# Performance work log

Hardware: AMD Instinct MI355X
Metric: run time of the kernel (lower is better)

Reference implementation:

```python
import jax, jax.numpy as jnp
import numpy as np

N, E = 50000, 800000
IN_DIM, HID, OUT = 64, 128, 64
EPS = 1e-5  # BatchNorm eps


def setup_inputs() -> dict:
    key = jax.random.key(0)
    ks = jax.random.split(key, 16)
    def w(k, i, o):
        return jax.random.normal(k, (i, o), jnp.float32) / np.float32(np.sqrt(i))
    def bn(k):
        km, kv = jax.random.split(k)
        return (jnp.ones((HID,), jnp.float32),                       # gamma
                jnp.zeros((HID,), jnp.float32),                      # beta
                0.1 * jax.random.normal(km, (HID,), jnp.float32),    # running mean
                0.5 + jax.random.uniform(kv, (HID,), jnp.float32))   # running var
    g0, be0, m0, v0 = bn(ks[6])
    g1, be1, m1, v1 = bn(ks[7])
    g2, be2, m2, v2 = bn(ks[8])
    return {
        "x":   jax.random.normal(ks[0], (N, IN_DIM), jnp.float32),
        "src": jax.random.randint(ks[1], (E,), 0, N, jnp.int32),
        "dst": jax.random.randint(ks[2], (E,), 0, N, jnp.int32),
        "W0": w(ks[3], IN_DIM, HID), "b0": jnp.zeros((HID,), jnp.float32),
        "g0": g0, "be0": be0, "m0": m0, "v0": v0,
        "W1": w(ks[4], HID, HID), "b1": jnp.zeros((HID,), jnp.float32),
        "g1": g1, "be1": be1, "m1": m1, "v1": v1,
        "W2": w(ks[5], HID, HID), "b2": jnp.zeros((HID,), jnp.float32),
        "g2": g2, "be2": be2, "m2": m2, "v2": v2,
        "Wm1": w(ks[9], HID, HID), "bm1": jnp.zeros((HID,), jnp.float32),
        "Wm2": w(ks[10], HID, OUT), "bm2": jnp.zeros((OUT,), jnp.float32),
    }


def gcn_conv(x, src, dst, W, b):
    # PyG GCNConv: h = x @ W; add self loops; symmetric normalization; scatter-add; + bias
    h = x @ W                                                     # [N, F]
    ones = jnp.ones((src.shape[0],), h.dtype)
    deg = 1.0 + jax.ops.segment_sum(ones, dst, num_segments=N)   # self loop adds 1
    dinv = jax.lax.rsqrt(deg)                                     # deg^-1/2 (deg >= 1)
    coef = (dinv[src] * dinv[dst])[:, None]                       # per-edge norm
    agg = jax.ops.segment_sum(h[src] * coef, dst, num_segments=N)
    return agg + h * (dinv * dinv)[:, None] + b                   # self-loop term + bias


def bn_relu(x, g, be, m, v):
    # eval-mode BatchNorm1d followed by ReLU (dropout is identity in eval)
    return jax.nn.relu((x - m) * jax.lax.rsqrt(v + EPS) * g + be)


def reference(x, src, dst,
              W0, b0, g0, be0, m0, v0,
              W1, b1, g1, be1, m1, v1,
              W2, b2, g2, be2, m2, v2,
              Wm1, bm1, Wm2, bm2):
    h = bn_relu(gcn_conv(x, src, dst, W0, b0), g0, be0, m0, v0)
    h = bn_relu(gcn_conv(h, src, dst, W1, b1), g1, be1, m1, v1)
    h = bn_relu(gcn_conv(h, src, dst, W2, b2), g2, be2, m2, v2)
    h = jax.nn.relu(h @ Wm1 + bm1)
    return h @ Wm2 + bm2
```

## Files before the change

### kernel.cpp

```cpp
#include <hip/hip_runtime.h>
#include <hip/hip_fp16.h>

#define BN_EPS 1e-5f
#define BK 512
#define NBMAX 128
#define ECH 8192
#define BCAP 9216
#define ECAP 64

typedef _Float16 half_t;
typedef _Float16 half8 __attribute__((ext_vector_type(8)));
typedef float floatx4 __attribute__((ext_vector_type(4)));


__global__ __launch_bounds__(256) void scatter_cvt_kernel(
    const int* __restrict__ src, const int* __restrict__ dst,
    int* __restrict__ bcursor, int2* __restrict__ tmp,
    const float* __restrict__ x, __half* __restrict__ x16,
    int E, int nb, int sb, int n4) {
  const int t = threadIdx.x;
  if (blockIdx.x >= sb) {
    int i = (blockIdx.x - sb) * 256 + t;
    if (i < n4) {
      float4 v = *(const float4*)(x + (size_t)i * 4);
      union { __half h[4]; float2 f; } u;
      u.h[0] = __float2half_rn(v.x);
      u.h[1] = __float2half_rn(v.y);
      u.h[2] = __float2half_rn(v.z);
      u.h[3] = __float2half_rn(v.w);
      *(float2*)(x16 + (size_t)i * 4) = u.f;
    }
    return;
  }
  __shared__ int h[NBMAX];
  for (int i = t; i < nb; i += 256) h[i] = 0;
  __syncthreads();
  const int base = blockIdx.x * ECH;
#pragma unroll 8
  for (int p = 0; p < ECH / 256; ++p) {
    int e = base + p * 256 + t;
    if (e < E) atomicAdd(&h[dst[e] >> 9], 1);
  }
  __syncthreads();
  for (int i = t; i < nb; i += 256) {
    int c = h[i];
    h[i] = c ? (i * BCAP + atomicAdd(&bcursor[i], c)) : 0;
  }
  __syncthreads();
#pragma unroll 8
  for (int p = 0; p < ECH / 256; ++p) {
    int e = base + p * 256 + t;
    if (e < E) {
      int s = src[e], d = dst[e];
      int pos = atomicAdd(&h[d >> 9], 1);
      tmp[pos] = make_int2(s, d);
    }
  }
}

__global__ __launch_bounds__(256) void bucket_finalize_kernel(
    const int2* __restrict__ tmp, const int* __restrict__ bcursor,
    int* __restrict__ offs, int* __restrict__ offe, float* __restrict__ dinv,
    int* __restrict__ esrc, __half* __restrict__ x16, int n) {
  __shared__ int deg[BK];
  __shared__ int cur[BK];
  __shared__ float fdi[BK];
  __shared__ int ts[256];
  const int t = threadIdx.x;
  const int b = blockIdx.x;
  const int nbase = b * BK;
  const int nn = min(BK, n - nbase);
  const int cnt = bcursor[b];
  const int2* tp = tmp + (size_t)b * BCAP;
  for (int i = t; i < nn; i += 256) deg[i] = 0;
  __syncthreads();
  for (int e = t; e < cnt; e += 256)
    atomicAdd(&deg[tp[e].y - nbase], 1);
  __syncthreads();
  int d0 = (2 * t < nn) ? deg[2 * t] : 0;
  int d1 = (2 * t + 1 < nn) ? deg[2 * t + 1] : 0;
  ts[t] = d0 + d1;
  __syncthreads();
  for (int o = 1; o < 256; o <<= 1) {
    int v = (t >= o) ? ts[t - o] : 0;
    __syncthreads();
    ts[t] += v;
    __syncthreads();
  }
  int base = b * BCAP + ((t == 0) ? 0 : ts[t - 1]);
  if (2 * t < nn) {
    float di = rsqrtf(1.0f + (float)d0);
    offs[nbase + 2 * t] = base;
    offe[nbase + 2 * t] = base + d0;
    cur[2 * t] = base;
    fdi[2 * t] = di;
    dinv[nbase + 2 * t] = di;
  }
  if (2 * t + 1 < nn) {
    float di = rsqrtf(1.0f + (float)d1);
    offs[nbase + 2 * t + 1] = base + d0;
    offe[nbase + 2 * t + 1] = base + d0 + d1;
    cur[2 * t + 1] = base + d0;
    fdi[2 * t + 1] = di;
    dinv[nbase + 2 * t + 1] = di;
  }
  __syncthreads();
  for (int e = t; e < cnt; e += 256) {
    int2 r = tp[e];
    int pos = atomicAdd(&cur[r.y - nbase], 1);
    esrc[pos] = r.x;
  }
  __half2* xp = (__half2*)x16;
  for (int i = t; i < nn * 32; i += 256) {
    int nl = i >> 5;
    size_t idx = (((size_t)(nbase + nl)) << 5) + (i & 31);
    float2 v = __half22float2(xp[idx]);
    float s = fdi[nl];
    xp[idx] = __floats2half2_rn(v.x * s, v.y * s);
  }
}


template <int FIN, int FOUT, int EPI, bool HALFOUT>
__global__ __launch_bounds__(256) void mgemm_kernel(
    const __half* __restrict__ X, const float* __restrict__ W,
    const float* __restrict__ bias, const float* __restrict__ gam,
    const float* __restrict__ bet, const float* __restrict__ mean,
    const float* __restrict__ var, void* __restrict__ Yv, int n) {
  constexpr int LDK = 72;
  constexpr int NCI = FOUT / 16;
  __shared__ half_t Asm[128 * LDK];
  __shared__ half_t Bsm[FOUT * LDK];

  const int t = threadIdx.x;
  const int wave = t >> 6, lane = t & 63;
  const int quad = lane >> 4, l16 = lane & 15;
  const int rowBase = blockIdx.x * 128;

  floatx4 acc[2][NCI];
#pragma unroll
  for (int i = 0; i < 2; ++i)
#pragma unroll
    for (int ci = 0; ci < NCI; ++ci) acc[i][ci] = (floatx4){0.f, 0.f, 0.f, 0.f};

  for (int kc = 0; kc < FIN; kc += 64) {
    __syncthreads();
    {
      const int kq = t & 15, m0 = t >> 4;
#pragma unroll
      for (int p = 0; p < 8; ++p) {
        int m = p * 16 + m0;
        int row = rowBase + m;
        uint2 v = make_uint2(0u, 0u);
        if (row < n) v = *(const uint2*)(X + (size_t)row * FIN + kc + kq * 4);
        *(uint2*)&Asm[m * LDK + kq * 4] = v;
      }
    }
    {
#pragma unroll
      for (int c0 = 0; c0 < FOUT * 16; c0 += 256) {
        int c = c0 + t;
        int nn = c % FOUT;
        int kg = (c / FOUT) * 4;
        const float* wp = W + (size_t)(kc + kg) * FOUT + nn;
        half_t* d = &Bsm[nn * LDK + kg];
        d[0] = (half_t)wp[0];
        d[1] = (half_t)wp[FOUT];
        d[2] = (half_t)wp[2 * FOUT];
        d[3] = (half_t)wp[3 * FOUT];
      }
    }
    __syncthreads();
#pragma unroll
    for (int kk = 0; kk < 2; ++kk) {
      half8 a0 = *(const half8*)&Asm[(wave * 32 + l16) * LDK + kk * 32 + quad * 8];
      half8 a1 = *(const half8*)&Asm[(wave * 32 + 16 + l16) * LDK + kk * 32 + quad * 8];
#pragma unroll
      for (int ci = 0; ci < NCI; ++ci) {
        half8 b = *(const half8*)&Bsm[(ci * 16 + l16) * LDK + kk * 32 + quad * 8];
        acc[0][ci] = __builtin_amdgcn_mfma_f32_16x16x32_f16(a0, b, acc[0][ci], 0, 0, 0);
        acc[1][ci] = __builtin_amdgcn_mfma_f32_16x16x32_f16(a1, b, acc[1][ci], 0, 0, 0);
      }
    }
  }

  float sc[NCI], sh[NCI];
#pragma unroll
  for (int ci = 0; ci < NCI; ++ci) {
    int col = ci * 16 + l16;
    if constexpr (EPI == 3) {
      float s = gam[col] * rsqrtf(var[col] + BN_EPS);
      sc[ci] = s;
      sh[ci] = (bias[col] - mean[col]) * s + bet[col];
    } else if constexpr (EPI == 1 || EPI == 2) {
      sc[ci] = 1.f;
      sh[ci] = bias[col];
    } else {
      sc[ci] = 1.f;
      sh[ci] = 0.f;
    }
  }
  float rs[2][4];
  if constexpr (EPI == 4) {
#pragma unroll
    for (int ri = 0; ri < 2; ++ri)
#pragma unroll
      for (int r = 0; r < 4; ++r) {
        int row = rowBase + wave * 32 + ri * 16 + quad * 4 + r;
        rs[ri][r] = (row < n) ? bias[row] : 0.f;
      }
  }
#pragma unroll
  for (int ri = 0; ri < 2; ++ri)
#pragma unroll
    for (int ci = 0; ci < NCI; ++ci) {
      int col = ci * 16 + l16;
#pragma unroll
      for (int r = 0; r < 4; ++r) {
        int row = rowBase + wave * 32 + ri * 16 + quad * 4 + r;
        if (row < n) {
          float v = acc[ri][ci][r];
          if constexpr (EPI == 4) v *= rs[ri][r];
          if constexpr (EPI == 1 || EPI == 2 || EPI == 3) v = fmaf(v, sc[ci], sh[ci]);
          if constexpr (EPI == 1 || EPI == 3) v = fmaxf(v, 0.f);
          if constexpr (HALFOUT)
            ((half_t*)Yv)[(size_t)row * FOUT + col] = (half_t)v;
          else
            ((float*)Yv)[(size_t)row * FOUT + col] = v;
        }
      }
    }
}


__global__ __launch_bounds__(256) void mlp_kernel(
    const __half* __restrict__ X, const float* __restrict__ W1,
    const float* __restrict__ b1f, const float* __restrict__ W2,
    const float* __restrict__ b2f, float* __restrict__ Y, int n) {
  constexpr int LDK = 72;
  constexpr int LDK2 = 136;
  __shared__ half_t smem[(128 + 64) * LDK2];
  half_t* As1 = smem;
  half_t* Bs1 = smem + 128 * LDK;
  half_t* As2 = smem;
  half_t* Bs2 = smem + 128 * LDK2;

  const int t = threadIdx.x;
  const int wave = t >> 6, lane = t & 63;
  const int quad = lane >> 4, l16 = lane & 15;
  const int rowBase = blockIdx.x * 128;

  floatx4 acc[2][8];
#pragma unroll
  for (int i = 0; i < 2; ++i)
#pragma unroll
    for (int ci = 0; ci < 8; ++ci) acc[i][ci] = (floatx4){0.f, 0.f, 0.f, 0.f};

  for (int kc = 0; kc < 128; kc += 64) {
    __syncthreads();
    {
      const int kq = t & 15, m0 = t >> 4;
#pragma unroll
      for (int p = 0; p < 8; ++p) {
        int m = p * 16 + m0;
        int row = rowBase + m;
        uint2 v = make_uint2(0u, 0u);
        if (row < n) v = *(const uint2*)(X + (size_t)row * 128 + kc + kq * 4);
        *(uint2*)&As1[m * LDK + kq * 4] = v;
      }
    }
    {
#pragma unroll
      for (int c0 = 0; c0 < 128 * 16; c0 += 256) {
        int c = c0 + t;
        int nn = c & 127;
        int kg = (c >> 7) << 2;
        const float* wp = W1 + (size_t)(kc + kg) * 128 + nn;
        half_t* d = &Bs1[nn * LDK + kg];
        d[0] = (half_t)wp[0];
        d[1] = (half_t)wp[128];
        d[2] = (half_t)wp[256];
        d[3] = (half_t)wp[384];
      }
    }
    __syncthreads();
#pragma unroll
    for (int kk = 0; kk < 2; ++kk) {
      half8 a0 = *(const half8*)&As1[(wave * 32 + l16) * LDK + kk * 32 + quad * 8];
      half8 a1 = *(const half8*)&As1[(wave * 32 + 16 + l16) * LDK + kk * 32 + quad * 8];
#pragma unroll
      for (int ci = 0; ci < 8; ++ci) {
        half8 b = *(const half8*)&Bs1[(ci * 16 + l16) * LDK + kk * 32 + quad * 8];
        acc[0][ci] = __builtin_amdgcn_mfma_f32_16x16x32_f16(a0, b, acc[0][ci], 0, 0, 0);
        acc[1][ci] = __builtin_amdgcn_mfma_f32_16x16x32_f16(a1, b, acc[1][ci], 0, 0, 0);
      }
    }
  }
  __syncthreads();

#pragma unroll
  for (int ri = 0; ri < 2; ++ri)
#pragma unroll
    for (int ci = 0; ci < 8; ++ci) {
      int col = ci * 16 + l16;
      float bz = b1f[col];
#pragma unroll
      for (int r = 0; r < 4; ++r) {
        int m = wave * 32 + ri * 16 + quad * 4 + r;
        As2[m * LDK2 + col] = (half_t)fmaxf(acc[ri][ci][r] + bz, 0.f);
      }
    }
  {
#pragma unroll
    for (int c0 = 0; c0 < 64 * 32; c0 += 256) {
      int c = c0 + t;
      int nn = c & 63;
      int kg = (c >> 6) << 2;
      const float* wp = W2 + (size_t)kg * 64 + nn;
      half_t* d = &Bs2[nn * LDK2 + kg];
      d[0] = (half_t)wp[0];
      d[1] = (half_t)wp[64];
      d[2] = (half_t)wp[128];
      d[3] = (half_t)wp[192];
    }
  }
  __syncthreads();

  floatx4 acc2[2][4];
#pragma unroll
  for (int i = 0; i < 2; ++i)
#pragma unroll
    for (int ci = 0; ci < 4; ++ci) acc2[i][ci] = (floatx4){0.f, 0.f, 0.f, 0.f};
#pragma unroll
  for (int kk = 0; kk < 4; ++kk) {
    half8 a0 = *(const half8*)&As2[(wave * 32 + l16) * LDK2 + kk * 32 + quad * 8];
    half8 a1 = *(const half8*)&As2[(wave * 32 + 16 + l16) * LDK2 + kk * 32 + quad * 8];
#pragma unroll
    for (int ci = 0; ci < 4; ++ci) {
      half8 b = *(const half8*)&Bs2[(ci * 16 + l16) * LDK2 + kk * 32 + quad * 8];
      acc2[0][ci] = __builtin_amdgcn_mfma_f32_16x16x32_f16(a0, b, acc2[0][ci], 0, 0, 0);
      acc2[1][ci] = __builtin_amdgcn_mfma_f32_16x16x32_f16(a1, b, acc2[1][ci], 0, 0, 0);
    }
  }
#pragma unroll
  for (int ri = 0; ri < 2; ++ri)
#pragma unroll
    for (int ci = 0; ci < 4; ++ci) {
      int col = ci * 16 + l16;
      float bz = b2f[col];
#pragma unroll
      for (int r = 0; r < 4; ++r) {
        int row = rowBase + wave * 32 + ri * 16 + quad * 4 + r;
        if (row < n) Y[(size_t)row * 64 + col] = acc2[ri][ci][r] + bz;
      }
    }
}


__global__ __launch_bounds__(256) void agg64_kernel(
    const __half* __restrict__ h, const int* __restrict__ offs,
    const int* __restrict__ offe, const int* __restrict__ esrc,
    const float* __restrict__ dinv, __half* __restrict__ out, int n) {
  __shared__ int eidx[4][ECAP];
  const int wid = threadIdx.x >> 6;
  int gi = blockIdx.x * 4 + wid;
  if (gi >= n) return;
  const int lane = threadIdx.x & 63;
  const int q = lane >> 4;
  const int j = lane & 15;
  const __half2* hp = (const __half2*)h;
  const float di = dinv[gi];
  const int e0 = offs[gi];
  const int e1 = offe[gi];
  const int deg = e1 - e0;
  const int dm = min(deg, ECAP);
  if (lane < dm) eidx[wid][lane] = esrc[e0 + lane];

  float ax = 0.f, ay = 0.f, az = 0.f, aw = 0.f;
  float bx = 0.f, by = 0.f, bz = 0.f, bw = 0.f;
  const int mm = dm - 1;
  for (int k = 0; k < dm; k += 16) {
    int i0 = k + q, i1 = k + 4 + q, i2 = k + 8 + q, i3 = k + 12 + q;
    int s0 = eidx[wid][min(i0, mm)];
    int s1 = eidx[wid][min(i1, mm)];
    int s2 = eidx[wid][min(i2, mm)];
    int s3 = eidx[wid][min(i3, mm)];
    uint2 r0 = *(const uint2*)(hp + (((size_t)s0) << 5) + j * 2);
    uint2 r1 = *(const uint2*)(hp + (((size_t)s1) << 5) + j * 2);
    uint2 r2 = *(const uint2*)(hp + (((size_t)s2) << 5) + j * 2);
    uint2 r3 = *(const uint2*)(hp + (((size_t)s3) << 5) + j * 2);
    if (i0 >= dm) { r0.x = 0u; r0.y = 0u; }
    if (i1 >= dm) { r1.x = 0u; r1.y = 0u; }
    if (i2 >= dm) { r2.x = 0u; r2.y = 0u; }
    if (i3 >= dm) { r3.x = 0u; r3.y = 0u; }
    float2 p0 = __half22float2(*(__half2*)&r0.x);
    float2 p1 = __half22float2(*(__half2*)&r0.y);
    float2 q0 = __half22float2(*(__half2*)&r1.x);
    float2 q1 = __half22float2(*(__half2*)&r1.y);
    float2 u0 = __half22float2(*(__half2*)&r2.x);
    float2 u1 = __half22float2(*(__half2*)&r2.y);
    float2 v0 = __half22float2(*(__half2*)&r3.x);
    float2 v1 = __half22float2(*(__half2*)&r3.y);
    ax += p0.x; ay += p0.y; az += p1.x; aw += p1.y;
    bx += q0.x; by += q0.y; bz += q1.x; bw += q1.y;
    ax += u0.x; ay += u0.y; az += u1.x; aw += u1.y;
    bx += v0.x; by += v0.y; bz += v1.x; bw += v1.y;
  }
  for (int e = e0 + ECAP; e < e1; e += 4) {
    int i0 = e + q;
    int s0 = esrc[min(i0, e1 - 1)];
    uint2 r0 = *(const uint2*)(hp + (((size_t)s0) << 5) + j * 2);
    if (i0 >= e1) { r0.x = 0u; r0.y = 0u; }
    float2 p0 = __half22float2(*(__half2*)&r0.x);
    float2 p1 = __half22float2(*(__half2*)&r0.y);
    ax += p0.x; ay += p0.y; az += p1.x; aw += p1.y;
  }
  ax += bx; ay += by; az += bz; aw += bw;
  ax += __shfl_xor(ax, 16); ay += __shfl_xor(ay, 16);
  az += __shfl_xor(az, 16); aw += __shfl_xor(aw, 16);
  ax += __shfl_xor(ax, 32); ay += __shfl_xor(ay, 32);
  az += __shfl_xor(az, 32); aw += __shfl_xor(aw, 32);
  if (q == 0) {
    uint2 rs = *(const uint2*)(hp + (((size_t)gi) << 5) + j * 2);
    float2 s0 = __half22float2(*(__half2*)&rs.x);
    float2 s1 = __half22float2(*(__half2*)&rs.y);
    __half2 h0 = __floats2half2_rn(di * (ax + s0.x), di * (ay + s0.y));
    __half2 h1 = __floats2half2_rn(di * (az + s1.x), di * (aw + s1.y));
    uint2 ov;
    ov.x = *(unsigned*)&h0;
    ov.y = *(unsigned*)&h1;
    *(uint2*)((__half2*)out + (((size_t)gi) << 5) + j * 2) = ov;
  }
}

__global__ __launch_bounds__(256) void agg128_bn_kernel(
    const __half* __restrict__ h, const int* __restrict__ offs,
    const int* __restrict__ offe, const int* __restrict__ esrc,
    const float* __restrict__ dinv,
    const float* __restrict__ bias, const float* __restrict__ gam,
    const float* __restrict__ bet, const float* __restrict__ mean,
    const float* __restrict__ var, __half* __restrict__ out, int n) {
  __shared__ int eidx[4][ECAP];
  const int wid = threadIdx.x >> 6;
  int gi = blockIdx.x * 4 + wid;
  if (gi >= n) return;
  const int lane = threadIdx.x & 63;
  const int hh = lane >> 5;
  const int j = lane & 31;
  const __half2* hp = (const __half2*)h;
  const float di = dinv[gi];
  const int e0 = offs[gi];
  const int e1 = offe[gi];
  const int deg = e1 - e0;
  const int dm = min(deg, ECAP);
  if (lane < dm) eidx[wid][lane] = esrc[e0 + lane];

  float ax = 0.f, ay = 0.f, az = 0.f, aw = 0.f;
  float bx = 0.f, by = 0.f, bz = 0.f, bw = 0.f;
  const int mm = dm - 1;
  for (int k = 0; k < dm; k += 8) {
    int i0 = k + hh, i1 = k + 2 + hh, i2 = k + 4 + hh, i3 = k + 6 + hh;
    int s0 = eidx[wid][min(i0, mm)];
    int s1 = eidx[wid][min(i1, mm)];
    int s2 = eidx[wid][min(i2, mm)];
    int s3 = eidx[wid][min(i3, mm)];
    uint2 r0 = *(const uint2*)(hp + (((size_t)s0) << 6) + j * 2);
    uint2 r1 = *(const uint2*)(hp + (((size_t)s1) << 6) + j * 2);
    uint2 r2 = *(const uint2*)(hp + (((size_t)s2) << 6) + j * 2);
    uint2 r3 = *(const uint2*)(hp + (((size_t)s3) << 6) + j * 2);
    if (i0 >= dm) { r0.x = 0u; r0.y = 0u; }
    if (i1 >= dm) { r1.x = 0u; r1.y = 0u; }
    if (i2 >= dm) { r2.x = 0u; r2.y = 0u; }
    if (i3 >= dm) { r3.x = 0u; r3.y = 0u; }
    float2 p0 = __half22float2(*(__half2*)&r0.x);
    float2 p1 = __half22float2(*(__half2*)&r0.y);
    float2 q0 = __half22float2(*(__half2*)&r1.x);
    float2 q1 = __half22float2(*(__half2*)&r1.y);
    float2 u0 = __half22float2(*(__half2*)&r2.x);
    float2 u1 = __half22float2(*(__half2*)&r2.y);
    float2 v0 = __half22float2(*(__half2*)&r3.x);
    float2 v1 = __half22float2(*(__half2*)&r3.y);
    ax += p0.x; ay += p0.y; az += p1.x; aw += p1.y;
    bx += q0.x; by += q0.y; bz += q1.x; bw += q1.y;
    ax += u0.x; ay += u0.y; az += u1.x; aw += u1.y;
    bx += v0.x; by += v0.y; bz += v1.x; bw += v1.y;
  }
  for (int e = e0 + ECAP; e < e1; e += 2) {
    int i0 = e + hh;
    int s0 = esrc[min(i0, e1 - 1)];
    uint2 r0 = *(const uint2*)(hp + (((size_t)s0) << 6) + j * 2);
    if (i0 >= e1) { r0.x = 0u; r0.y = 0u; }
    float2 p0 = __half22float2(*(__half2*)&r0.x);
    float2 p1 = __half22float2(*(__half2*)&r0.y);
    ax += p0.x; ay += p0.y; az += p1.x; aw += p1.y;
  }
  ax += bx; ay += by; az += bz; aw += bw;
  ax += __shfl_xor(ax, 32); ay += __shfl_xor(ay, 32);
  az += __shfl_xor(az, 32); aw += __shfl_xor(aw, 32);
  if (hh == 0) {
    uint2 rs = *(const uint2*)(hp + (((size_t)gi) << 6) + j * 2);
    float2 s0 = __half22float2(*(__half2*)&rs.x);
    float2 s1 = __half22float2(*(__half2*)&rs.y);
    float v0 = di * (ax + s0.x);
    float v1 = di * (ay + s0.y);
    float v2 = di * (az + s1.x);
    float v3 = di * (aw + s1.y);
    const int c = j * 4;
    float4 bv = *(const float4*)(bias + c);
    float4 gv = *(const float4*)(gam + c);
    float4 bev = *(const float4*)(bet + c);
    float4 mv = *(const float4*)(mean + c);
    float4 vv = *(const float4*)(var + c);
    float o0 = fmaxf(fmaf(v0 + bv.x - mv.x, gv.x * rsqrtf(vv.x + BN_EPS), bev.x), 0.f);
    float o1 = fmaxf(fmaf(v1 + bv.y - mv.y, gv.y * rsqrtf(vv.y + BN_EPS), bev.y), 0.f);
    float o2 = fmaxf(fmaf(v2 + bv.z - mv.z, gv.z * rsqrtf(vv.z + BN_EPS), bev.z), 0.f);
    float o3 = fmaxf(fmaf(v3 + bv.w - mv.w, gv.w * rsqrtf(vv.w + BN_EPS), bev.w), 0.f);
    __half2 h0 = __floats2half2_rn(o0, o1);
    __half2 h1 = __floats2half2_rn(o2, o3);
    uint2 ov;
    ov.x = *(unsigned*)&h0;
    ov.y = *(unsigned*)&h1;
    *(uint2*)((__half2*)out + (((size_t)gi) << 6) + j * 2) = ov;
  }
}


static inline size_t alignup(size_t x, size_t a) { return (x + a - 1) & ~(a - 1); }

extern "C" void kernel_launch(void* const* d_in, const int* in_sizes, int n_in,
                              void* d_out, int out_size, void* d_ws, size_t ws_size,
                              hipStream_t stream) {
  const float* x   = (const float*)d_in[0];
  const int*   src = (const int*)d_in[1];
  const int*   dst = (const int*)d_in[2];
  const float* W0  = (const float*)d_in[3];
  const float* b0  = (const float*)d_in[4];
  const float* g0  = (const float*)d_in[5];
  const float* be0 = (const float*)d_in[6];
  const float* m0  = (const float*)d_in[7];
  const float* v0  = (const float*)d_in[8];
  const float* W1  = (const float*)d_in[9];
  const float* b1  = (const float*)d_in[10];
  const float* g1  = (const float*)d_in[11];
  const float* be1 = (const float*)d_in[12];
  const float* m1  = (const float*)d_in[13];
  const float* v1  = (const float*)d_in[14];
  const float* W2  = (const float*)d_in[15];
  const float* b2  = (const float*)d_in[16];
  const float* g2  = (const float*)d_in[17];
  const float* be2 = (const float*)d_in[18];
  const float* m2  = (const float*)d_in[19];
  const float* v2  = (const float*)d_in[20];
  const float* Wm1 = (const float*)d_in[21];
  const float* bm1 = (const float*)d_in[22];
  const float* Wm2 = (const float*)d_in[23];
  const float* bm2 = (const float*)d_in[24];

  const int N = in_sizes[0] / 64;
  const int E = in_sizes[1];

  char* p = (char*)d_ws;
  auto take = [&](size_t bytes) {
    char* r = p;
    p += alignup(bytes, 256);
    return r;
  };
  const int nbk = (N + BK - 1) / BK;
  int*    bcursor= (int*)take(NBMAX * 4);
  int*    offs   = (int*)take((size_t)N * 4);
  int*    offe   = (int*)take((size_t)N * 4);
  float*  dinv   = (float*)take((size_t)N * 4);
  int*    esrc   = (int*)take((size_t)nbk * BCAP * 4);
  int2*   tmp    = (int2*)take((size_t)nbk * BCAP * 8);
  __half* x16    = (__half*)take((size_t)N * 64 * 2);
  __half* aggx16 = (__half*)take((size_t)N * 64 * 2);
  __half* t0     = (__half*)take((size_t)N * 128 * 2);
  __half* t1     = (__half*)take((size_t)N * 128 * 2);
  float*  yout   = (float*)d_out;

  const int TB = 256;
  const int sb = (E + ECH - 1) / ECH;
  const int n4 = N * 16;
  const int cb = (n4 + 255) / 256;

  hipMemsetAsync(bcursor, 0, NBMAX * 4, stream);
  scatter_cvt_kernel<<<sb + cb, TB, 0, stream>>>(src, dst, bcursor, tmp,
                                                 x, x16, E, nbk, sb, n4);
  bucket_finalize_kernel<<<nbk, TB, 0, stream>>>(tmp, bcursor, offs, offe,
                                                 dinv, esrc, x16, N);

  const int gemmGrid = (N + 127) / 128;
  const int aggGrid = (N + 3) / 4;

  agg64_kernel<<<aggGrid, TB, 0, stream>>>(x16, offs, offe, esrc, dinv, aggx16, N);
  mgemm_kernel<64, 128, 3, true><<<gemmGrid, TB, 0, stream>>>(
      aggx16, W0, b0, g0, be0, m0, v0, t0, N);
  mgemm_kernel<128, 128, 4, true><<<gemmGrid, TB, 0, stream>>>(
      t0, W1, dinv, nullptr, nullptr, nullptr, nullptr, t1, N);
  agg128_bn_kernel<<<aggGrid, TB, 0, stream>>>(t1, offs, offe, esrc, dinv,
                                               b1, g1, be1, m1, v1, t0, N);
  mgemm_kernel<128, 128, 4, true><<<gemmGrid, TB, 0, stream>>>(
      t0, W2, dinv, nullptr, nullptr, nullptr, nullptr, t1, N);
  agg128_bn_kernel<<<aggGrid, TB, 0, stream>>>(t1, offs, offe, esrc, dinv,
                                               b2, g2, be2, m2, v2, t0, N);
  mlp_kernel<<<gemmGrid, TB, 0, stream>>>(t0, Wm1, bm1, Wm2, bm2, yout, N);
}
```

Before: 315.3 us.

## Pack bucketed edges into 32-bit words and unroll aggregation gathers by eight

Bucketed edge records are packed into a single 32-bit word (src shifted left by 9, OR'd with the local dst index) instead of an int2. This halves the temporary edge buffer traffic in the scatter and finalize kernels. The aggregation kernels gain an unbounded fast path that issues eight gathers per iteration with no masking when at least a full batch of neighbors remains, keeping more loads in flight. The packing relies on src fitting in 23 bits, and the wider unroll adds register pressure.

Measured after the change: 312.5 us, median of 2. About the same (-0.9%).

```diff
diff --git a/kernel.cpp b/kernel.cpp
--- a/kernel.cpp
+++ b/kernel.cpp
@@ -15,7 +15,7 @@
 
 __global__ __launch_bounds__(256) void scatter_cvt_kernel(
     const int* __restrict__ src, const int* __restrict__ dst,
-    int* __restrict__ bcursor, int2* __restrict__ tmp,
+    int* __restrict__ bcursor, unsigned* __restrict__ tmp,
     const float* __restrict__ x, __half* __restrict__ x16,
     int E, int nb, int sb, int n4) {
   const int t = threadIdx.x;
@@ -53,13 +53,13 @@
     if (e < E) {
       int s = src[e], d = dst[e];
       int pos = atomicAdd(&h[d >> 9], 1);
-      tmp[pos] = make_int2(s, d);
+      tmp[pos] = ((unsigned)s << 9) | (unsigned)(d & 511);
     }
   }
 }
 
 __global__ __launch_bounds__(256) void bucket_finalize_kernel(
-    const int2* __restrict__ tmp, const int* __restrict__ bcursor,
+    const unsigned* __restrict__ tmp, const int* __restrict__ bcursor,
     int* __restrict__ offs, int* __restrict__ offe, float* __restrict__ dinv,
     int* __restrict__ esrc, __half* __restrict__ x16, int n) {
   __shared__ int deg[BK];
@@ -71,11 +71,11 @@
   const int nbase = b * BK;
   const int nn = min(BK, n - nbase);
   const int cnt = bcursor[b];
-  const int2* tp = tmp + (size_t)b * BCAP;
+  const unsigned* tp = tmp + (size_t)b * BCAP;
   for (int i = t; i < nn; i += 256) deg[i] = 0;
   __syncthreads();
   for (int e = t; e < cnt; e += 256)
-    atomicAdd(&deg[tp[e].y - nbase], 1);
+    atomicAdd(&deg[tp[e] & 511u], 1);
   __syncthreads();
   int d0 = (2 * t < nn) ? deg[2 * t] : 0;
   int d1 = (2 * t + 1 < nn) ? deg[2 * t + 1] : 0;
@@ -106,9 +106,9 @@
   }
   __syncthreads();
   for (int e = t; e < cnt; e += 256) {
-    int2 r = tp[e];
-    int pos = atomicAdd(&cur[r.y - nbase], 1);
-    esrc[pos] = r.x;
+    unsigned r = tp[e];
+    int pos = atomicAdd(&cur[r & 511u], 1);
+    esrc[pos] = (int)(r >> 9);
   }
   __half2* xp = (__half2*)x16;
   for (int i = t; i < nn * 32; i += 256) {
@@ -378,8 +378,44 @@
 
   float ax = 0.f, ay = 0.f, az = 0.f, aw = 0.f;
   float bx = 0.f, by = 0.f, bz = 0.f, bw = 0.f;
+  int k = 0;
+  for (; k + 32 <= dm; k += 32) {
+    int s0 = eidx[wid][k + q];
+    int s1 = eidx[wid][k + 4 + q];
+    int s2 = eidx[wid][k + 8 + q];
+    int s3 = eidx[wid][k + 12 + q];
+    int s4 = eidx[wid][k + 16 + q];
+    int s5 = eidx[wid][k + 20 + q];
+    int s6 = eidx[wid][k + 24 + q];
+    int s7 = eidx[wid][k + 28 + q];
+    uint2 r0 = *(const uint2*)(hp + (((size_t)s0) << 5) + j * 2);
+    uint2 r1 = *(const uint2*)(hp + (((size_t)s1) << 5) + j * 2);
+    uint2 r2 = *(const uint2*)(hp + (((size_t)s2) << 5) + j * 2);
+    uint2 r3 = *(const uint2*)(hp + (((size_t)s3) << 5) + j * 2);
+    uint2 r4 = *(const uint2*)(hp + (((size_t)s4) << 5) + j * 2);
+    uint2 r5 = *(const uint2*)(hp + (((size_t)s5) << 5) + j * 2);
+    uint2 r6 = *(const uint2*)(hp + (((size_t)s6) << 5) + j * 2);
+    uint2 r7 = *(const uint2*)(hp + (((size_t)s7) << 5) + j * 2);
+    float2 f;
+    f = __half22float2(*(__half2*)&r0.x); ax += f.x; ay += f.y;
+    f = __half22float2(*(__half2*)&r0.y); az += f.x; aw += f.y;
+    f = __half22float2(*(__half2*)&r1.x); bx += f.x; by += f.y;
+    f = __half22float2(*(__half2*)&r1.y); bz += f.x; bw += f.y;
+    f = __half22float2(*(__half2*)&r2.x); ax += f.x; ay += f.y;
+    f = __half22float2(*(__half2*)&r2.y); az += f.x; aw += f.y;
+    f = __half22float2(*(__half2*)&r3.x); bx += f.x; by += f.y;
+    f = __half22float2(*(__half2*)&r3.y); bz += f.x; bw += f.y;
+    f = __half22float2(*(__half2*)&r4.x); ax += f.x; ay += f.y;
+    f = __half22float2(*(__half2*)&r4.y); az += f.x; aw += f.y;
+    f = __half22float2(*(__half2*)&r5.x); bx += f.x; by += f.y;
+    f = __half22float2(*(__half2*)&r5.y); bz += f.x; bw += f.y;
+    f = __half22float2(*(__half2*)&r6.x); ax += f.x; ay += f.y;
+    f = __half22float2(*(__half2*)&r6.y); az += f.x; aw += f.y;
+    f = __half22float2(*(__half2*)&r7.x); bx += f.x; by += f.y;
+    f = __half22float2(*(__half2*)&r7.y); bz += f.x; bw += f.y;
+  }
   const int mm = dm - 1;
-  for (int k = 0; k < dm; k += 16) {
+  for (; k < dm; k += 16) {
     int i0 = k + q, i1 = k + 4 + q, i2 = k + 8 + q, i3 = k + 12 + q;
     int s0 = eidx[wid][min(i0, mm)];
     int s1 = eidx[wid][min(i1, mm)];
@@ -393,27 +429,24 @@
     if (i1 >= dm) { r1.x = 0u; r1.y = 0u; }
     if (i2 >= dm) { r2.x = 0u; r2.y = 0u; }
     if (i3 >= dm) { r3.x = 0u; r3.y = 0u; }
-    float2 p0 = __half22float2(*(__half2*)&r0.x);
-    float2 p1 = __half22float2(*(__half2*)&r0.y);
-    float2 q0 = __half22float2(*(__half2*)&r1.x);
-    float2 q1 = __half22float2(*(__half2*)&r1.y);
-    float2 u0 = __half22float2(*(__half2*)&r2.x);
-    float2 u1 = __half22float2(*(__half2*)&r2.y);
-    float2 v0 = __half22float2(*(__half2*)&r3.x);
-    float2 v1 = __half22float2(*(__half2*)&r3.y);
-    ax += p0.x; ay += p0.y; az += p1.x; aw += p1.y;
-    bx += q0.x; by += q0.y; bz += q1.x; bw += q1.y;
-    ax += u0.x; ay += u0.y; az += u1.x; aw += u1.y;
-    bx += v0.x; by += v0.y; bz += v1.x; bw += v1.y;
+    float2 f;
+    f = __half22float2(*(__half2*)&r0.x); ax += f.x; ay += f.y;
+    f = __half22float2(*(__half2*)&r0.y); az += f.x; aw += f.y;
+    f = __half22float2(*(__half2*)&r1.x); bx += f.x; by += f.y;
+    f = __half22float2(*(__half2*)&r1.y); bz += f.x; bw += f.y;
+    f = __half22float2(*(__half2*)&r2.x); ax += f.x; ay += f.y;
+    f = __half22float2(*(__half2*)&r2.y); az += f.x; aw += f.y;
+    f = __half22float2(*(__half2*)&r3.x); bx += f.x; by += f.y;
+    f = __half22float2(*(__half2*)&r3.y); bz += f.x; bw += f.y;
   }
   for (int e = e0 + ECAP; e < e1; e += 4) {
     int i0 = e + q;
     int s0 = esrc[min(i0, e1 - 1)];
     uint2 r0 = *(const uint2*)(hp + (((size_t)s0) << 5) + j * 2);
     if (i0 >= e1) { r0.x = 0u; r0.y = 0u; }
-    float2 p0 = __half22float2(*(__half2*)&r0.x);
-    float2 p1 = __half22float2(*(__half2*)&r0.y);
-    ax += p0.x; ay += p0.y; az += p1.x; aw += p1.y;
+    float2 f;
+    f = __half22float2(*(__half2*)&r0.x); ax += f.x; ay += f.y;
+    f = __half22float2(*(__half2*)&r0.y); az += f.x; aw += f.y;
   }
   ax += bx; ay += by; az += bz; aw += bw;
   ax += __shfl_xor(ax, 16); ay += __shfl_xor(ay, 16);
@@ -457,8 +490,44 @@
 
   float ax = 0.f, ay = 0.f, az = 0.f, aw = 0.f;
   float bx = 0.f, by = 0.f, bz = 0.f, bw = 0.f;
+  int k = 0;
+  for (; k + 16 <= dm; k += 16) {
+    int s0 = eidx[wid][k + hh];
+    int s1 = eidx[wid][k + 2 + hh];
+    int s2 = eidx[wid][k + 4 + hh];
+    int s3 = eidx[wid][k + 6 + hh];
+    int s4 = eidx[wid][k + 8 + hh];
+    int s5 = eidx[wid][k + 10 + hh];
+    int s6 = eidx[wid][k + 12 + hh];
+    int s7 = eidx[wid][k + 14 + hh];
+    uint2 r0 = *(const uint2*)(hp + (((size_t)s0) << 6) + j * 2);
+    uint2 r1 = *(const uint2*)(hp + (((size_t)s1) << 6) + j * 2);
+    uint2 r2 = *(const uint2*)(hp + (((size_t)s2) << 6) + j * 2);
+    uint2 r3 = *(const uint2*)(hp + (((size_t)s3) << 6) + j * 2);
+    uint2 r4 = *(const uint2*)(hp + (((size_t)s4) << 6) + j * 2);
+    uint2 r5 = *(const uint2*)(hp + (((size_t)s5) << 6) + j * 2);
+    uint2 r6 = *(const uint2*)(hp + (((size_t)s6) << 6) + j * 2);
+    uint2 r7 = *(const uint2*)(hp + (((size_t)s7) << 6) + j * 2);
+    float2 f;
+    f = __half22float2(*(__half2*)&r0.x); ax += f.x; ay += f.y;
+    f = __half22float2(*(__half2*)&r0.y); az += f.x; aw += f.y;
+    f = __half22float2(*(__half2*)&r1.x); bx += f.x; by += f.y;
+    f = __half22float2(*(__half2*)&r1.y); bz += f.x; bw += f.y;
+    f = __half22float2(*(__half2*)&r2.x); ax += f.x; ay += f.y;
+    f = __half22float2(*(__half2*)&r2.y); az += f.x; aw += f.y;
+    f = __half22float2(*(__half2*)&r3.x); bx += f.x; by += f.y;
+    f = __half22float2(*(__half2*)&r3.y); bz += f.x; bw += f.y;
+    f = __half22float2(*(__half2*)&r4.x); ax += f.x; ay += f.y;
+    f = __half22float2(*(__half2*)&r4.y); az += f.x; aw += f.y;
+    f = __half22float2(*(__half2*)&r5.x); bx += f.x; by += f.y;
+    f = __half22float2(*(__half2*)&r5.y); bz += f.x; bw += f.y;
+    f = __half22float2(*(__half2*)&r6.x); ax += f.x; ay += f.y;
+    f = __half22float2(*(__half2*)&r6.y); az += f.x; aw += f.y;
+    f = __half22float2(*(__half2*)&r7.x); bx += f.x; by += f.y;
+    f = __half22float2(*(__half2*)&r7.y); bz += f.x; bw += f.y;
+  }
   const int mm = dm - 1;
-  for (int k = 0; k < dm; k += 8) {
+  for (; k < dm; k += 8) {
     int i0 = k + hh, i1 = k + 2 + hh, i2 = k + 4 + hh, i3 = k + 6 + hh;
     int s0 = eidx[wid][min(i0, mm)];
     int s1 = eidx[wid][min(i1, mm)];
@@ -472,27 +541,24 @@
     if (i1 >= dm) { r1.x = 0u; r1.y = 0u; }
     if (i2 >= dm) { r2.x = 0u; r2.y = 0u; }
     if (i3 >= dm) { r3.x = 0u; r3.y = 0u; }
-    float2 p0 = __half22float2(*(__half2*)&r0.x);
-    float2 p1 = __half22float2(*(__half2*)&r0.y);
-    float2 q0 = __half22float2(*(__half2*)&r1.x);
-    float2 q1 = __half22float2(*(__half2*)&r1.y);
-    float2 u0 = __half22float2(*(__half2*)&r2.x);
-    float2 u1 = __half22float2(*(__half2*)&r2.y);
-    float2 v0 = __half22float2(*(__half2*)&r3.x);
-    float2 v1 = __half22float2(*(__half2*)&r3.y);
-    ax += p0.x; ay += p0.y; az += p1.x; aw += p1.y;
-    bx += q0.x; by += q0.y; bz += q1.x; bw += q1.y;
-    ax += u0.x; ay += u0.y; az += u1.x; aw += u1.y;
-    bx += v0.x; by += v0.y; bz += v1.x; bw += v1.y;
+    float2 f;
+    f = __half22float2(*(__half2*)&r0.x); ax += f.x; ay += f.y;
+    f = __half22float2(*(__half2*)&r0.y); az += f.x; aw += f.y;
+    f = __half22float2(*(__half2*)&r1.x); bx += f.x; by += f.y;
+    f = __half22float2(*(__half2*)&r1.y); bz += f.x; bw += f.y;
+    f = __half22float2(*(__half2*)&r2.x); ax += f.x; ay += f.y;
+    f = __half22float2(*(__half2*)&r2.y); az += f.x; aw += f.y;
+    f = __half22float2(*(__half2*)&r3.x); bx += f.x; by += f.y;
+    f = __half22float2(*(__half2*)&r3.y); bz += f.x; bw += f.y;
   }
   for (int e = e0 + ECAP; e < e1; e += 2) {
     int i0 = e + hh;
     int s0 = esrc[min(i0, e1 - 1)];
     uint2 r0 = *(const uint2*)(hp + (((size_t)s0) << 6) + j * 2);
     if (i0 >= e1) { r0.x = 0u; r0.y = 0u; }
-    float2 p0 = __half22float2(*(__half2*)&r0.x);
-    float2 p1 = __half22float2(*(__half2*)&r0.y);
-    ax += p0.x; ay += p0.y; az += p1.x; aw += p1.y;
+    float2 f;
+    f = __half22float2(*(__half2*)&r0.x); ax += f.x; ay += f.y;
+    f = __half22float2(*(__half2*)&r0.y); az += f.x; aw += f.y;
   }
   ax += bx; ay += by; az += bz; aw += bw;
   ax += __shfl_xor(ax, 32); ay += __shfl_xor(ay, 32);
@@ -566,17 +632,17 @@
     return r;
   };
   const int nbk = (N + BK - 1) / BK;
-  int*    bcursor= (int*)take(NBMAX * 4);
-  int*    offs   = (int*)take((size_t)N * 4);
-  int*    offe   = (int*)take((size_t)N * 4);
-  float*  dinv   = (float*)take((size_t)N * 4);
-  int*    esrc   = (int*)take((size_t)nbk * BCAP * 4);
-  int2*   tmp    = (int2*)take((size_t)nbk * BCAP * 8);
-  __half* x16    = (__half*)take((size_t)N * 64 * 2);
-  __half* aggx16 = (__half*)take((size_t)N * 64 * 2);
-  __half* t0     = (__half*)take((size_t)N * 128 * 2);
-  __half* t1     = (__half*)take((size_t)N * 128 * 2);
-  float*  yout   = (float*)d_out;
+  int*      bcursor= (int*)take(NBMAX * 4);
+  int*      offs   = (int*)take((size_t)N * 4);
+  int*      offe   = (int*)take((size_t)N * 4);
+  float*    dinv   = (float*)take((size_t)N * 4);
+  int*      esrc   = (int*)take((size_t)nbk * BCAP * 4);
+  unsigned* tmp    = (unsigned*)take((size_t)nbk * BCAP * 4);
+  __half*   x16    = (__half*)take((size_t)N * 64 * 2);
+  __half*   aggx16 = (__half*)take((size_t)N * 64 * 2);
+  __half*   t0     = (__half*)take((size_t)N * 128 * 2);
+  __half*   t1     = (__half*)take((size_t)N * 128 * 2);
+  float*    yout   = (float*)d_out;
 
   const int TB = 256;
   const int sb = (E + ECH - 1) / ECH;
```
